# Kernel tuning notes

Hardware: AMD Instinct MI355X
Metric: run time of the kernel (lower is better)

## Reference

```python
import jax, jax.numpy as jnp
import numpy as np

LABEL_SMOOTHING = 0.1
SAMPLE_SIZE = 512
VOCAB = 50257


def setup_inputs() -> dict:
    key = jax.random.key(0)
    k1, k2, k3, k4 = jax.random.split(key, 4)
    B, S, H = 2, 512, 768
    N = B * S
    hidden_states = jax.random.normal(k1, (B, S, H), dtype=jnp.float32)
    weight = jax.random.normal(k2, (VOCAB, H), dtype=jnp.float32)
    target = jax.random.randint(k3, (B, S), 0, VOCAB, dtype=jnp.int64)
    noise_indx = jax.random.randint(k4, (N, SAMPLE_SIZE), 0, VOCAB, dtype=jnp.int64)
    return {"hidden_states": hidden_states, "weight": weight,
            "target": target, "noise_indx": noise_indx}


def reference(hidden_states, weight, target, noise_indx):
    B, S, H = hidden_states.shape
    h = hidden_states.reshape(-1, H)            # [N, H]
    t = target.reshape(-1)                      # [N]  (all valid: no -100)

    # target logit: dot(h_n, W[t_n])
    logits_target = jnp.sum(h * weight[t], axis=-1)              # [N]
    # noise logits: gather 512 rows per token, batched matvec
    logits_noise = jnp.einsum('nsh,nh->ns', weight[noise_indx], h)  # [N, 512]

    all_logits = jnp.concatenate([logits_target[:, None], logits_noise], axis=-1)  # [N, 513]
    lsm = jax.nn.log_softmax(all_logits, axis=-1)

    target_prob = 1.0 - LABEL_SMOOTHING
    noise_prob = LABEL_SMOOTHING / SAMPLE_SIZE
    loss = -target_prob * lsm[:, 0] - noise_prob * jnp.sum(lsm[:, 1:], axis=-1)
    return loss.mean()
```

## Files before the change

kernel.cpp:

```cpp
#include <hip/hip_runtime.h>
#include <math.h>

#define HDIM   768
#define NSAMP  512
#define NLOG   513
#define VOCAB  50257
#define PADV   53248


__device__ __forceinline__ unsigned int bf16rn(float x)
{
    unsigned int u = __float_as_uint(x);
    return (u + 0x7fffu + ((u >> 16) & 1u)) >> 16;
}
__device__ __forceinline__ float blo(unsigned int u) { return __uint_as_float(u << 16); }
__device__ __forceinline__ float bhi(unsigned int u) { return __uint_as_float(u & 0xffff0000u); }

#define CONVB 128
#define HISTB 384
__global__ __launch_bounds__(256) void pre_kernel(
    const float* __restrict__ h, unsigned int* __restrict__ hb,
    const int* __restrict__ target, const int* __restrict__ noise,
    unsigned int* __restrict__ counts, int N, int nhu)
{
    if (blockIdx.x < CONVB) {
        int i = blockIdx.x * 256 + threadIdx.x;
        const int stride = CONVB * 256;
        for (; i < nhu; i += stride) {
            const int row = i / 384;
            const int q   = i - row * 384;
            const int k = q >> 6, r = q & 63;
            const int p = r >> 2, jj = r & 3;
            const int m = 24 * p + 4 * k + jj;
            const float2 pr = reinterpret_cast<const float2*>(h)[(size_t)row * 384 + m];
            hb[i] = bf16rn(pr.x) | (bf16rn(pr.y) << 16);
        }
    } else {
        int i = (blockIdx.x - CONVB) * 256 + threadIdx.x;
        const int stride = HISTB * 256;
        const int nn4 = (N * NSAMP) / 4;
        const int4* noise4 = reinterpret_cast<const int4*>(noise);
        for (int kk = i; kk < nn4; kk += stride) {
            const int4 vv = noise4[kk];
            atomicAdd(&counts[vv.x], 1u);
            atomicAdd(&counts[vv.y], 1u);
            atomicAdd(&counts[vv.z], 1u);
            atomicAdd(&counts[vv.w], 1u);
        }
        for (int kk = i; kk < N; kk += stride) atomicAdd(&counts[target[kk]], 1u);
    }
}

__global__ __launch_bounds__(1024) void scan_kernel(
    const unsigned int* __restrict__ counts, unsigned int* __restrict__ cursor)
{
    const int tid = threadIdx.x;
    const uint4* c4 = reinterpret_cast<const uint4*>(counts) + tid * 13;
    uint4*      o4 = reinterpret_cast<uint4*>(cursor) + tid * 13;

    __shared__ unsigned int lds[1024];
    unsigned int s = 0;
    #pragma unroll
    for (int i = 0; i < 13; ++i) {
        const uint4 c = c4[i];
        s += c.x + c.y + c.z + c.w;
    }
    lds[tid] = s;
    __syncthreads();
    #pragma unroll
    for (int off = 1; off < 1024; off <<= 1) {
        unsigned int t = (tid >= off) ? lds[tid - off] : 0u;
        __syncthreads();
        lds[tid] += t;
        __syncthreads();
    }
    unsigned int run = (tid > 0) ? lds[tid - 1] : 0u;
    #pragma unroll
    for (int i = 0; i < 13; ++i) {
        const uint4 c = c4[i];
        uint4 o;
        o.x = run;
        o.y = o.x + c.x;
        o.z = o.y + c.y;
        o.w = o.z + c.z;
        run = o.w + c.w;
        o4[i] = o;
    }
}

__global__ __launch_bounds__(256) void scatter_kernel(
    const int* __restrict__ target, const int* __restrict__ noise,
    unsigned int* __restrict__ cursor,
    unsigned int* __restrict__ sorted_pay, int N)
{
    int i = blockIdx.x * 256 + threadIdx.x;
    int stride = gridDim.x * 256;
    const int nn4 = (N * NSAMP) / 4;
    const int4* noise4 = reinterpret_cast<const int4*>(noise);
    for (int k = i; k < nn4; k += stride) {
        const int4 vv = noise4[k];
        const int kk = k * 4;
        #pragma unroll
        for (int j = 0; j < 4; ++j) {
            const int v    = (j == 0) ? vv.x : (j == 1) ? vv.y : (j == 2) ? vv.z : vv.w;
            const int idx  = kk + j;
            const int tok  = idx >> 9;
            const int slot = (idx & 511) + 1;
            const unsigned int pos = atomicAdd(&cursor[v], 1u);
            sorted_pay[pos] = ((unsigned int)tok << 10) | (unsigned int)slot;
        }
    }
    for (int k = i; k < N; k += stride) {
        const int v = target[k];
        const unsigned int pos = atomicAdd(&cursor[v], 1u);
        sorted_pay[pos] = ((unsigned int)k << 10);
    }
}

#define DOT8(X, WA, WB) \
    (blo(X.x)*WA.x + bhi(X.x)*WA.y + blo(X.y)*WA.z + bhi(X.y)*WA.w + \
     blo(X.z)*WB.x + bhi(X.z)*WB.y + blo(X.w)*WB.z + bhi(X.w)*WB.w)

#define GTPB 256
__global__ __launch_bounds__(GTPB) void gather_run_kernel(
    const unsigned int* __restrict__ hb,
    const float* __restrict__ W,
    const unsigned int* __restrict__ counts,
    const unsigned int* __restrict__ cursor,
    const unsigned int* __restrict__ sorted_pay,
    float* __restrict__ logits)
{
    const int v = blockIdx.x * (GTPB / 64) + (threadIdx.x >> 6);
    if (v >= VOCAB) return;
    const int cnt = (int)counts[v];
    if (cnt == 0) return;
    const int start = (int)cursor[v] - cnt;
    const int lane  = threadIdx.x & 63;
    const int p     = lane & 15;
    const int g     = lane >> 4;
    const int last  = cnt - 1;

    const float4* wr = reinterpret_cast<const float4*>(W + (size_t)v * HDIM);
    float4 wf[12];
    #pragma unroll
    for (int k = 0; k < 12; ++k) wf[k] = wr[12 * p + k];

    const unsigned int* sp = sorted_pay + start;

    int idx0 = (g < last) ? g : last;
    unsigned int pay = sp[idx0];
    const uint4* hr = reinterpret_cast<const uint4*>(hb) + (size_t)(pay >> 10) * 96;
    uint4 x0 = hr[p],      x1 = hr[p + 16], x2 = hr[p + 32],
          x3 = hr[p + 48], x4 = hr[p + 64], x5 = hr[p + 80];

    for (int j = 0; j < cnt; j += 4) {
        const int jn  = j + 4 + g;
        const int idn = (jn < last) ? jn : last;
        const unsigned int payn = sp[idn];
        const uint4* hn = reinterpret_cast<const uint4*>(hb) + (size_t)(payn >> 10) * 96;
        const uint4 n0 = hn[p],      n1 = hn[p + 16], n2 = hn[p + 32],
                    n3 = hn[p + 48], n4 = hn[p + 64], n5 = hn[p + 80];

        float s;
        s  = DOT8(x0, wf[0],  wf[1]);
        s += DOT8(x1, wf[2],  wf[3]);
        s += DOT8(x2, wf[4],  wf[5]);
        s += DOT8(x3, wf[6],  wf[7]);
        s += DOT8(x4, wf[8],  wf[9]);
        s += DOT8(x5, wf[10], wf[11]);

        #pragma unroll
        for (int off = 8; off; off >>= 1) s += __shfl_xor(s, off, 64);

        if (p == 0 && j + g <= last)
            logits[(size_t)(pay >> 10) * NLOG + (pay & 1023u)] = s;

        pay = payn;
        x0 = n0; x1 = n1; x2 = n2; x3 = n3; x4 = n4; x5 = n5;
    }
}

__global__ __launch_bounds__(256) void softmax_loss_kernel(
    const float* __restrict__ logits, float* __restrict__ loss_per_token)
{
    const int n    = blockIdx.x;
    const int tid  = threadIdx.x;
    const int lane = tid & 63;
    const int wave = tid >> 6;
    const float* row = logits + (size_t)n * NLOG;

    __shared__ float red[4];
    __shared__ float red2[4][2];

    float lmax = -INFINITY;
    for (int r = tid; r < NLOG; r += 256) lmax = fmaxf(lmax, row[r]);
    #pragma unroll
    for (int off = 32; off; off >>= 1) lmax = fmaxf(lmax, __shfl_xor(lmax, off, 64));
    if (lane == 0) red[wave] = lmax;
    __syncthreads();
    lmax = fmaxf(fmaxf(red[0], red[1]), fmaxf(red[2], red[3]));

    float esum = 0.f, lsum = 0.f;
    for (int r = tid; r < NLOG; r += 256) {
        const float l = row[r];
        esum += __expf(l - lmax);
        if (r > 0) lsum += l;
    }
    #pragma unroll
    for (int off = 32; off; off >>= 1) {
        esum += __shfl_xor(esum, off, 64);
        lsum += __shfl_xor(lsum, off, 64);
    }
    if (lane == 0) { red2[wave][0] = esum; red2[wave][1] = lsum; }
    __syncthreads();

    if (tid == 0) {
        esum = red2[0][0] + red2[1][0] + red2[2][0] + red2[3][0];
        lsum = red2[0][1] + red2[1][1] + red2[2][1] + red2[3][1];
        const float lse  = lmax + logf(esum);
        const float l0   = row[0];
        const float loss = -0.9f * (l0 - lse)
                         - (0.1f / 512.f) * (lsum - 512.f * lse);
        loss_per_token[n] = loss;
    }
}

__global__ __launch_bounds__(256) void reduce_mean_kernel(
    const float* __restrict__ x, float* __restrict__ out, int n)
{
    const int tid = threadIdx.x;
    float s = 0.f;
    for (int i = tid; i < n; i += 256) s += x[i];
    #pragma unroll
    for (int off = 32; off; off >>= 1) s += __shfl_xor(s, off, 64);
    __shared__ float red[4];
    if ((tid & 63) == 0) red[tid >> 6] = s;
    __syncthreads();
    if (tid == 0) out[0] = (red[0] + red[1] + red[2] + red[3]) / (float)n;
}

__global__ __launch_bounds__(512) void nce_token_kernel(
    const float* __restrict__ h, const float* __restrict__ W,
    const int* __restrict__ target, const int* __restrict__ noise,
    float* __restrict__ loss_per_token)
{
    const int n    = blockIdx.x;
    const int tid  = threadIdx.x;
    const int lane = tid & 63;
    const int wave = tid >> 6;

    __shared__ float  logits[NLOG];
    __shared__ float4 hsm[HDIM / 4];
    __shared__ float  red[8];
    __shared__ float  red2[8][2];

    const float4* hrow = reinterpret_cast<const float4*>(h + (size_t)n * HDIM);
    if (tid < HDIM / 4) hsm[tid] = hrow[tid];
    __syncthreads();

    const float4 h0 = hsm[lane];
    const float4 h1 = hsm[lane + 64];
    const float4 h2 = hsm[lane + 128];
    const int* nrow = noise + (size_t)n * NSAMP;

    for (int r = wave; r < NLOG; r += 8) {
        const int row = (r == 0) ? target[n] : nrow[r - 1];
        const float4* wr = reinterpret_cast<const float4*>(W + (size_t)row * HDIM);
        const float4 w0 = wr[lane];
        const float4 w1 = wr[lane + 64];
        const float4 w2 = wr[lane + 128];
        float s;
        s  = h0.x * w0.x + h0.y * w0.y + h0.z * w0.z + h0.w * w0.w;
        s += h1.x * w1.x + h1.y * w1.y + h1.z * w1.z + h1.w * w1.w;
        s += h2.x * w2.x + h2.y * w2.y + h2.z * w2.z + h2.w * w2.w;
        #pragma unroll
        for (int off = 32; off; off >>= 1) s += __shfl_xor(s, off, 64);
        if (lane == 0) logits[r] = s;
    }
    __syncthreads();

    float lmax = -INFINITY;
    for (int r = tid; r < NLOG; r += 512) lmax = fmaxf(lmax, logits[r]);
    #pragma unroll
    for (int off = 32; off; off >>= 1) lmax = fmaxf(lmax, __shfl_xor(lmax, off, 64));
    if (lane == 0) red[wave] = lmax;
    __syncthreads();
    if (wave == 0) {
        float m = (lane < 8) ? red[lane] : -INFINITY;
        #pragma unroll
        for (int off = 4; off; off >>= 1) m = fmaxf(m, __shfl_xor(m, off, 64));
        if (lane == 0) red[0] = m;
    }
    __syncthreads();
    lmax = red[0];

    float esum = 0.f, lsum = 0.f;
    for (int r = tid; r < NLOG; r += 512) {
        const float l = logits[r];
        esum += __expf(l - lmax);
        if (r > 0) lsum += l;
    }
    #pragma unroll
    for (int off = 32; off; off >>= 1) {
        esum += __shfl_xor(esum, off, 64);
        lsum += __shfl_xor(lsum, off, 64);
    }
    if (lane == 0) { red2[wave][0] = esum; red2[wave][1] = lsum; }
    __syncthreads();

    if (tid == 0) {
        esum = 0.f; lsum = 0.f;
        #pragma unroll
        for (int w = 0; w < 8; ++w) { esum += red2[w][0]; lsum += red2[w][1]; }
        const float lse  = lmax + logf(esum);
        const float loss = -0.9f * (logits[0] - lse)
                         - (0.1f / 512.f) * (lsum - 512.f * lse);
        loss_per_token[n] = loss;
    }
}

extern "C" void kernel_launch(void* const* d_in, const int* in_sizes, int n_in,
                              void* d_out, int out_size, void* d_ws, size_t ws_size,
                              hipStream_t stream)
{
    const float* h      = (const float*)d_in[0];
    const float* W      = (const float*)d_in[1];
    const int*   target = (const int*)d_in[2];
    const int*   noise  = (const int*)d_in[3];
    float*       out    = (float*)d_out;
    const int    N      = in_sizes[2];
    const int    nocc   = N * NLOG;
    const int    nh2    = N * HDIM / 2;

    unsigned int* counts     = (unsigned int*)d_ws;
    unsigned int* cursor     = counts + PADV;
    unsigned int* sorted_pay = cursor + PADV;
    unsigned int* hb         = sorted_pay + nocc;
    float*        logits     = (float*)(hb + nh2);
    float*        loss       = logits + nocc;
    const size_t  need_bytes = (size_t)(2 * PADV + 2 * nocc + nh2 + N) * 4;

    if (ws_size < need_bytes) {
        float* ws = (float*)d_ws;
        nce_token_kernel<<<N, 512, 0, stream>>>(h, W, target, noise, ws);
        reduce_mean_kernel<<<1, 256, 0, stream>>>(ws, out, N);
        return;
    }

    hipMemsetAsync(counts, 0, (size_t)PADV * 4, stream);
    pre_kernel<<<CONVB + HISTB, 256, 0, stream>>>(h, hb, target, noise,
                                                  counts, N, nh2);
    scan_kernel<<<1, 1024, 0, stream>>>(counts, cursor);
    scatter_kernel<<<512, 256, 0, stream>>>(target, noise, cursor, sorted_pay, N);
    const int gblocks = (VOCAB + (GTPB / 64) - 1) / (GTPB / 64);
    gather_run_kernel<<<gblocks, GTPB, 0, stream>>>(hb, W, counts, cursor,
                                                    sorted_pay, logits);
    softmax_loss_kernel<<<N, 256, 0, stream>>>(logits, loss);
    reduce_mean_kernel<<<1, 256, 0, stream>>>(loss, out, N);
}
```

Before: 164.6 us.

## Switch gather dot products to fp16 packed dot2 with full-wave rows

Converts hidden states to fp16 instead of bf16 and packs each vocab weight row to fp16 in registers, so the gather kernel can use the packed fdot2 instruction in place of scalar bf16 unpack-and-FMA sequences. The thread mapping changes from four tokens per wave with 16 lanes each to one token per full 64-lane wave, with two tokens processed per iteration and a two-deep prefetch pipeline. The hidden-state layout permutation in the pre-kernel goes away because each lane now reads contiguous chunks. This cuts ALU work and register pressure from the 48-float weight array. The cost is fp16 range and precision risk for the weights and activations, plus a longer 64-wide shuffle reduction.

```diff
diff --git a/kernel.cpp b/kernel.cpp
--- a/kernel.cpp
+++ b/kernel.cpp
@@ -1,4 +1,5 @@
 #include <hip/hip_runtime.h>
+#include <hip/hip_fp16.h>
 #include <math.h>
 
 #define HDIM   768
@@ -8,13 +9,26 @@
 #define PADV   53248
 
 
-__device__ __forceinline__ unsigned int bf16rn(float x)
-{
-    unsigned int u = __float_as_uint(x);
-    return (u + 0x7fffu + ((u >> 16) & 1u)) >> 16;
-}
-__device__ __forceinline__ float blo(unsigned int u) { return __uint_as_float(u << 16); }
-__device__ __forceinline__ float bhi(unsigned int u) { return __uint_as_float(u & 0xffff0000u); }
+typedef _Float16 h2_t __attribute__((ext_vector_type(2)));
+
+__device__ __forceinline__ unsigned int pkh(float x, float y)
+{
+    const unsigned lo = __half_as_ushort(__float2half_rn(x));
+    const unsigned hi = __half_as_ushort(__float2half_rn(y));
+    return lo | (hi << 16);
+}
+
+__device__ __forceinline__ float dot2(unsigned int a, unsigned int b, float c)
+{
+#if __has_builtin(__builtin_amdgcn_fdot2)
+    return __builtin_amdgcn_fdot2(__builtin_bit_cast(h2_t, a),
+                                  __builtin_bit_cast(h2_t, b), c, false);
+#else
+    const h2_t ha = __builtin_bit_cast(h2_t, a);
+    const h2_t hb = __builtin_bit_cast(h2_t, b);
+    return c + (float)ha.x * (float)hb.x + (float)ha.y * (float)hb.y;
+#endif
+}
 
 #define CONVB 128
 #define HISTB 384
@@ -27,13 +41,8 @@
         int i = blockIdx.x * 256 + threadIdx.x;
         const int stride = CONVB * 256;
         for (; i < nhu; i += stride) {
-            const int row = i / 384;
-            const int q   = i - row * 384;
-            const int k = q >> 6, r = q & 63;
-            const int p = r >> 2, jj = r & 3;
-            const int m = 24 * p + 4 * k + jj;
-            const float2 pr = reinterpret_cast<const float2*>(h)[(size_t)row * 384 + m];
-            hb[i] = bf16rn(pr.x) | (bf16rn(pr.y) << 16);
+            const float2 pr = reinterpret_cast<const float2*>(h)[i];
+            hb[i] = pkh(pr.x, pr.y);
         }
     } else {
         int i = (blockIdx.x - CONVB) * 256 + threadIdx.x;
@@ -117,10 +126,6 @@
     }
 }
 
-#define DOT8(X, WA, WB) \
-    (blo(X.x)*WA.x + bhi(X.x)*WA.y + blo(X.y)*WA.z + bhi(X.y)*WA.w + \
-     blo(X.z)*WB.x + bhi(X.z)*WB.y + blo(X.w)*WB.z + bhi(X.w)*WB.w)
-
 #define GTPB 256
 __global__ __launch_bounds__(GTPB) void gather_run_kernel(
     const unsigned int* __restrict__ hb,
@@ -136,48 +141,68 @@
     if (cnt == 0) return;
     const int start = (int)cursor[v] - cnt;
     const int lane  = threadIdx.x & 63;
-    const int p     = lane & 15;
-    const int g     = lane >> 4;
     const int last  = cnt - 1;
 
     const float4* wr = reinterpret_cast<const float4*>(W + (size_t)v * HDIM);
-    float4 wf[12];
-    #pragma unroll
-    for (int k = 0; k < 12; ++k) wf[k] = wr[12 * p + k];
+    const float4 a0 = wr[2 * lane], a1 = wr[2 * lane + 1], a2 = wr[128 + lane];
+    const unsigned wp0 = pkh(a0.x, a0.y), wp1 = pkh(a0.z, a0.w),
+                   wp2 = pkh(a1.x, a1.y), wp3 = pkh(a1.z, a1.w),
+                   wp4 = pkh(a2.x, a2.y), wp5 = pkh(a2.z, a2.w);
 
     const unsigned int* sp = sorted_pay + start;
-
-    int idx0 = (g < last) ? g : last;
-    unsigned int pay = sp[idx0];
-    const uint4* hr = reinterpret_cast<const uint4*>(hb) + (size_t)(pay >> 10) * 96;
-    uint4 x0 = hr[p],      x1 = hr[p + 16], x2 = hr[p + 32],
-          x3 = hr[p + 48], x4 = hr[p + 64], x5 = hr[p + 80];
-
-    for (int j = 0; j < cnt; j += 4) {
-        const int jn  = j + 4 + g;
-        const int idn = (jn < last) ? jn : last;
-        const unsigned int payn = sp[idn];
-        const uint4* hn = reinterpret_cast<const uint4*>(hb) + (size_t)(payn >> 10) * 96;
-        const uint4 n0 = hn[p],      n1 = hn[p + 16], n2 = hn[p + 32],
-                    n3 = hn[p + 48], n4 = hn[p + 64], n5 = hn[p + 80];
-
-        float s;
-        s  = DOT8(x0, wf[0],  wf[1]);
-        s += DOT8(x1, wf[2],  wf[3]);
-        s += DOT8(x2, wf[4],  wf[5]);
-        s += DOT8(x3, wf[6],  wf[7]);
-        s += DOT8(x4, wf[8],  wf[9]);
-        s += DOT8(x5, wf[10], wf[11]);
-
-        #pragma unroll
-        for (int off = 8; off; off >>= 1) s += __shfl_xor(s, off, 64);
-
-        if (p == 0 && j + g <= last)
-            logits[(size_t)(pay >> 10) * NLOG + (pay & 1023u)] = s;
-
-        pay = payn;
-        x0 = n0; x1 = n1; x2 = n2; x3 = n3; x4 = n4; x5 = n5;
-    }
+    #define CLMP(k) ((k) < last ? (k) : last)
+
+    unsigned pay0 = sp[0];
+    unsigned pay1 = sp[CLMP(1)];
+    unsigned pay2 = sp[CLMP(2)];
+    unsigned pay3 = sp[CLMP(3)];
+    const unsigned* r0 = hb + (size_t)(pay0 >> 10) * 384;
+    const unsigned* r1 = hb + (size_t)(pay1 >> 10) * 384;
+    const unsigned* r2 = hb + (size_t)(pay2 >> 10) * 384;
+    const unsigned* r3 = hb + (size_t)(pay3 >> 10) * 384;
+    uint4 x0 = reinterpret_cast<const uint4*>(r0)[lane];
+    uint2 y0 = reinterpret_cast<const uint2*>(r0 + 256)[lane];
+    uint4 x1 = reinterpret_cast<const uint4*>(r1)[lane];
+    uint2 y1 = reinterpret_cast<const uint2*>(r1 + 256)[lane];
+    uint4 x2 = reinterpret_cast<const uint4*>(r2)[lane];
+    uint2 y2 = reinterpret_cast<const uint2*>(r2 + 256)[lane];
+    uint4 x3 = reinterpret_cast<const uint4*>(r3)[lane];
+    uint2 y3 = reinterpret_cast<const uint2*>(r3 + 256)[lane];
+
+    for (int j = 0; j < cnt; j += 2) {
+        const unsigned payn0 = sp[CLMP(j + 4)];
+        const unsigned payn1 = sp[CLMP(j + 5)];
+        const unsigned* rn0 = hb + (size_t)(payn0 >> 10) * 384;
+        const unsigned* rn1 = hb + (size_t)(payn1 >> 10) * 384;
+        const uint4 nx0 = reinterpret_cast<const uint4*>(rn0)[lane];
+        const uint2 ny0 = reinterpret_cast<const uint2*>(rn0 + 256)[lane];
+        const uint4 nx1 = reinterpret_cast<const uint4*>(rn1)[lane];
+        const uint2 ny1 = reinterpret_cast<const uint2*>(rn1 + 256)[lane];
+
+        float s0a = dot2(x0.x, wp0, 0.f), s1a = dot2(x1.x, wp0, 0.f);
+        float s0b = dot2(x0.y, wp1, 0.f), s1b = dot2(x1.y, wp1, 0.f);
+        s0a = dot2(x0.z, wp2, s0a);  s1a = dot2(x1.z, wp2, s1a);
+        s0b = dot2(x0.w, wp3, s0b);  s1b = dot2(x1.w, wp3, s1b);
+        s0a = dot2(y0.x, wp4, s0a);  s1a = dot2(y1.x, wp4, s1a);
+        s0b = dot2(y0.y, wp5, s0b);  s1b = dot2(y1.y, wp5, s1b);
+        float s0 = s0a + s0b, s1 = s1a + s1b;
+
+        #pragma unroll
+        for (int off = 32; off; off >>= 1) {
+            s0 += __shfl_xor(s0, off, 64);
+            s1 += __shfl_xor(s1, off, 64);
+        }
+        if (lane == 0) {
+            logits[(size_t)(pay0 >> 10) * NLOG + (pay0 & 1023u)] = s0;
+            if (j + 1 < cnt)
+                logits[(size_t)(pay1 >> 10) * NLOG + (pay1 & 1023u)] = s1;
+        }
+
+        pay0 = pay2; pay1 = pay3; pay2 = payn0; pay3 = payn1;
+        x0 = x2; y0 = y2; x1 = x3; y1 = y3;
+        x2 = nx0; y2 = ny0; x3 = nx1; y3 = ny1;
+    }
+    #undef CLMP
 }
 
 __global__ __launch_bounds__(256) void softmax_loss_kernel(
```

Result: faster. 153.4 us (-6.8%).

## Compute gathered dot products with fp16 MFMA over sorted occurrence chunks

Applied to the files above, without the earlier changes.

Replaces the per-vocab-row wave gather kernel with a kernel where each wave takes 16 consecutive sorted occurrences. It computes a 16x16 MFMA tile over the full hidden dimension and keeps only the diagonal entries. Hidden states are now packed as fp16 in natural order instead of permuted bf16, and W rows are converted to fp16 on the fly. This removes the per-vocab load imbalance and the scalar FMA reduction, but computes 16x redundant products. It also reloads W per occurrence rather than once per vocab row, relying on the sort order for cache hits, and fp16 conversion may reduce accuracy or overflow.

```diff
diff --git a/kernel.cpp b/kernel.cpp
--- a/kernel.cpp
+++ b/kernel.cpp
@@ -1,4 +1,5 @@
 #include <hip/hip_runtime.h>
+#include <hip/hip_fp16.h>
 #include <math.h>
 
 #define HDIM   768
@@ -8,13 +9,16 @@
 #define PADV   53248
 
 
-__device__ __forceinline__ unsigned int bf16rn(float x)
-{
-    unsigned int u = __float_as_uint(x);
-    return (u + 0x7fffu + ((u >> 16) & 1u)) >> 16;
-}
-__device__ __forceinline__ float blo(unsigned int u) { return __uint_as_float(u << 16); }
-__device__ __forceinline__ float bhi(unsigned int u) { return __uint_as_float(u & 0xffff0000u); }
+typedef _Float16 f16x2 __attribute__((ext_vector_type(2)));
+typedef _Float16 f16x8 __attribute__((ext_vector_type(8)));
+typedef float    f32x4 __attribute__((ext_vector_type(4)));
+
+__device__ __forceinline__ unsigned int pkh(float x, float y)
+{
+    const unsigned lo = __half_as_ushort(__float2half_rn(x));
+    const unsigned hi = __half_as_ushort(__float2half_rn(y));
+    return lo | (hi << 16);
+}
 
 #define CONVB 128
 #define HISTB 384
@@ -27,13 +31,8 @@
         int i = blockIdx.x * 256 + threadIdx.x;
         const int stride = CONVB * 256;
         for (; i < nhu; i += stride) {
-            const int row = i / 384;
-            const int q   = i - row * 384;
-            const int k = q >> 6, r = q & 63;
-            const int p = r >> 2, jj = r & 3;
-            const int m = 24 * p + 4 * k + jj;
-            const float2 pr = reinterpret_cast<const float2*>(h)[(size_t)row * 384 + m];
-            hb[i] = bf16rn(pr.x) | (bf16rn(pr.y) << 16);
+            const float2 pr = reinterpret_cast<const float2*>(h)[i];
+            hb[i] = pkh(pr.x, pr.y);
         }
     } else {
         int i = (blockIdx.x - CONVB) * 256 + threadIdx.x;
@@ -91,7 +90,8 @@
 __global__ __launch_bounds__(256) void scatter_kernel(
     const int* __restrict__ target, const int* __restrict__ noise,
     unsigned int* __restrict__ cursor,
-    unsigned int* __restrict__ sorted_pay, int N)
+    unsigned int* __restrict__ sorted_pay,
+    unsigned short* __restrict__ sorted_v16, int N)
 {
     int i = blockIdx.x * 256 + threadIdx.x;
     int stride = gridDim.x * 256;
@@ -108,75 +108,63 @@
             const int slot = (idx & 511) + 1;
             const unsigned int pos = atomicAdd(&cursor[v], 1u);
             sorted_pay[pos] = ((unsigned int)tok << 10) | (unsigned int)slot;
+            sorted_v16[pos] = (unsigned short)v;
         }
     }
     for (int k = i; k < N; k += stride) {
         const int v = target[k];
         const unsigned int pos = atomicAdd(&cursor[v], 1u);
         sorted_pay[pos] = ((unsigned int)k << 10);
-    }
-}
-
-#define DOT8(X, WA, WB) \
-    (blo(X.x)*WA.x + bhi(X.x)*WA.y + blo(X.y)*WA.z + bhi(X.y)*WA.w + \
-     blo(X.z)*WB.x + bhi(X.z)*WB.y + blo(X.w)*WB.z + bhi(X.w)*WB.w)
+        sorted_v16[pos] = (unsigned short)v;
+    }
+}
 
 #define GTPB 256
-__global__ __launch_bounds__(GTPB) void gather_run_kernel(
+__global__ __launch_bounds__(GTPB) void mfma_chunk_kernel(
     const unsigned int* __restrict__ hb,
     const float* __restrict__ W,
-    const unsigned int* __restrict__ counts,
-    const unsigned int* __restrict__ cursor,
     const unsigned int* __restrict__ sorted_pay,
-    float* __restrict__ logits)
-{
-    const int v = blockIdx.x * (GTPB / 64) + (threadIdx.x >> 6);
-    if (v >= VOCAB) return;
-    const int cnt = (int)counts[v];
-    if (cnt == 0) return;
-    const int start = (int)cursor[v] - cnt;
+    const unsigned short* __restrict__ sorted_v16,
+    float* __restrict__ logits, int nocc)
+{
+    const int chunk = blockIdx.x * (GTPB / 64) + (threadIdx.x >> 6);
     const int lane  = threadIdx.x & 63;
-    const int p     = lane & 15;
-    const int g     = lane >> 4;
-    const int last  = cnt - 1;
-
-    const float4* wr = reinterpret_cast<const float4*>(W + (size_t)v * HDIM);
-    float4 wf[12];
-    #pragma unroll
-    for (int k = 0; k < 12; ++k) wf[k] = wr[12 * p + k];
-
-    const unsigned int* sp = sorted_pay + start;
-
-    int idx0 = (g < last) ? g : last;
-    unsigned int pay = sp[idx0];
-    const uint4* hr = reinterpret_cast<const uint4*>(hb) + (size_t)(pay >> 10) * 96;
-    uint4 x0 = hr[p],      x1 = hr[p + 16], x2 = hr[p + 32],
-          x3 = hr[p + 48], x4 = hr[p + 64], x5 = hr[p + 80];
-
-    for (int j = 0; j < cnt; j += 4) {
-        const int jn  = j + 4 + g;
-        const int idn = (jn < last) ? jn : last;
-        const unsigned int payn = sp[idn];
-        const uint4* hn = reinterpret_cast<const uint4*>(hb) + (size_t)(payn >> 10) * 96;
-        const uint4 n0 = hn[p],      n1 = hn[p + 16], n2 = hn[p + 32],
-                    n3 = hn[p + 48], n4 = hn[p + 64], n5 = hn[p + 80];
-
-        float s;
-        s  = DOT8(x0, wf[0],  wf[1]);
-        s += DOT8(x1, wf[2],  wf[3]);
-        s += DOT8(x2, wf[4],  wf[5]);
-        s += DOT8(x3, wf[6],  wf[7]);
-        s += DOT8(x4, wf[8],  wf[9]);
-        s += DOT8(x5, wf[10], wf[11]);
-
-        #pragma unroll
-        for (int off = 8; off; off >>= 1) s += __shfl_xor(s, off, 64);
-
-        if (p == 0 && j + g <= last)
-            logits[(size_t)(pay >> 10) * NLOG + (pay & 1023u)] = s;
-
-        pay = payn;
-        x0 = n0; x1 = n1; x2 = n2; x3 = n3; x4 = n4; x5 = n5;
+    const int q     = lane & 15;
+    const int kb    = lane >> 4;
+
+    int occ = chunk * 16 + q;
+    const bool valid = occ < nocc;
+    if (occ >= nocc) occ = nocc - 1;
+
+    const unsigned pay = sorted_pay[occ];
+    const unsigned v   = sorted_v16[occ];
+
+    const uint4*  hr4 = reinterpret_cast<const uint4*>(hb + (size_t)(pay >> 10) * 384);
+    const float4* wr4 = reinterpret_cast<const float4*>(W + (size_t)v * HDIM);
+
+    f32x4 acc = {0.f, 0.f, 0.f, 0.f};
+
+    #pragma unroll
+    for (int step = 0; step < 24; ++step) {
+        const uint4 a = hr4[step * 4 + kb];
+        const f16x8 af = __builtin_bit_cast(f16x8, a);
+        const float4 w0 = wr4[step * 8 + kb * 2];
+        const float4 w1 = wr4[step * 8 + kb * 2 + 1];
+        uint4 bu;
+        bu.x = __builtin_bit_cast(unsigned, __builtin_amdgcn_cvt_pkrtz(w0.x, w0.y));
+        bu.y = __builtin_bit_cast(unsigned, __builtin_amdgcn_cvt_pkrtz(w0.z, w0.w));
+        bu.z = __builtin_bit_cast(unsigned, __builtin_amdgcn_cvt_pkrtz(w1.x, w1.y));
+        bu.w = __builtin_bit_cast(unsigned, __builtin_amdgcn_cvt_pkrtz(w1.z, w1.w));
+        const f16x8 bf = __builtin_bit_cast(f16x8, bu);
+
+        acc = __builtin_amdgcn_mfma_f32_16x16x32_f16(af, bf, acc, 0, 0, 0);
+    }
+
+    if (valid && (lane >> 4) == (q >> 2)) {
+        const int r = q & 3;
+        const float val = (r == 0) ? acc[0] : (r == 1) ? acc[1]
+                        : (r == 2) ? acc[2] : acc[3];
+        logits[(size_t)(pay >> 10) * NLOG + (pay & 1023u)] = val;
     }
 }
 
@@ -332,13 +320,15 @@
     const int    nocc   = N * NLOG;
     const int    nh2    = N * HDIM / 2;
 
-    unsigned int* counts     = (unsigned int*)d_ws;
-    unsigned int* cursor     = counts + PADV;
-    unsigned int* sorted_pay = cursor + PADV;
-    unsigned int* hb         = sorted_pay + nocc;
-    float*        logits     = (float*)(hb + nh2);
-    float*        loss       = logits + nocc;
-    const size_t  need_bytes = (size_t)(2 * PADV + 2 * nocc + nh2 + N) * 4;
+    unsigned int*   counts     = (unsigned int*)d_ws;
+    unsigned int*   cursor     = counts + PADV;
+    unsigned int*   sorted_pay = cursor + PADV;
+    unsigned short* sorted_v16 = (unsigned short*)(sorted_pay + nocc);
+    unsigned int*   hb         = sorted_pay + nocc + (nocc + 1) / 2;
+    float*          logits     = (float*)(hb + nh2);
+    float*          loss       = logits + nocc;
+    const size_t    need_bytes = (size_t)(2 * PADV + nocc + (nocc + 1) / 2
+                                          + nh2 + nocc + N) * 4;
 
     if (ws_size < need_bytes) {
         float* ws = (float*)d_ws;
@@ -351,10 +341,12 @@
     pre_kernel<<<CONVB + HISTB, 256, 0, stream>>>(h, hb, target, noise,
                                                   counts, N, nh2);
     scan_kernel<<<1, 1024, 0, stream>>>(counts, cursor);
-    scatter_kernel<<<512, 256, 0, stream>>>(target, noise, cursor, sorted_pay, N);
-    const int gblocks = (VOCAB + (GTPB / 64) - 1) / (GTPB / 64);
-    gather_run_kernel<<<gblocks, GTPB, 0, stream>>>(hb, W, counts, cursor,
-                                                    sorted_pay, logits);
+    scatter_kernel<<<512, 256, 0, stream>>>(target, noise, cursor,
+                                            sorted_pay, sorted_v16, N);
+    const int chunks  = (nocc + 15) / 16;
+    const int gblocks = (chunks + (GTPB / 64) - 1) / (GTPB / 64);
+    mfma_chunk_kernel<<<gblocks, GTPB, 0, stream>>>(hb, W, sorted_pay,
+                                                    sorted_v16, logits, nocc);
     softmax_loss_kernel<<<N, 256, 0, stream>>>(logits, loss);
     reduce_mean_kernel<<<1, 256, 0, stream>>>(loss, out, N);
 }
```

After: 230.8 us. 40.2% more time.
